# Kernel tuning notes

Hardware: AMD Instinct MI355X
Metric: run time of the kernel (lower is better)

## Reference

```python
import jax, jax.numpy as jnp
import numpy as np

N = 100000
E = 1600000
D_IN = 128
D_H = 128


def _sage_conv(x, src, dst, W_self, W_neigh, b, n_nodes):
    # mean aggregation over in-neighbors: dst receives from src
    gathered = x[src]                                        # [E, D]
    summed = jax.ops.segment_sum(gathered, dst, num_segments=n_nodes)  # [N, D]
    deg = jax.ops.segment_sum(jnp.ones((src.shape[0],), x.dtype), dst,
                              num_segments=n_nodes)          # [N]
    mean_neigh = summed / jnp.maximum(deg, 1.0)[:, None]     # zero-degree -> 0
    return x @ W_self + mean_neigh @ W_neigh + b


def setup_inputs() -> dict:
    key = jax.random.key(0)
    ks = jax.random.split(key, 9)
    s1 = 1.0 / np.sqrt(D_IN)
    s2 = 1.0 / np.sqrt(D_H)
    return {
        "in_feat": jax.random.normal(ks[0], (N, D_IN), jnp.float32),
        "W1_self": jax.random.uniform(ks[1], (D_IN, D_H), jnp.float32, -s1, s1),
        "W1_neigh": jax.random.uniform(ks[2], (D_IN, D_H), jnp.float32, -s1, s1),
        "b1": jnp.zeros((D_H,), jnp.float32),
        "W2_self": jax.random.uniform(ks[3], (D_H, D_H), jnp.float32, -s2, s2),
        "W2_neigh": jax.random.uniform(ks[4], (D_H, D_H), jnp.float32, -s2, s2),
        "b2": jnp.zeros((D_H,), jnp.float32),
        "src": jax.random.randint(ks[5], (E,), 0, N, jnp.int32),
        "dst": jax.random.randint(ks[6], (E,), 0, N, jnp.int32),
    }


def reference(in_feat, W1_self, W1_neigh, b1, W2_self, W2_neigh, b2, src, dst):
    h = _sage_conv(in_feat, src, dst, W1_self, W1_neigh, b1, N)
    h = jax.nn.relu(h)
    h = _sage_conv(h, src, dst, W2_self, W2_neigh, b2, N)
    return h
```

## Files before the change

kernel.cpp:

```cpp
#include <hip/hip_runtime.h>
#include <hip/hip_fp16.h>

#define D 128
#define NB_MAX 1024
#define PART_BLOCKS 512
#define CNT_BLOCKS 512

using f32x4  = __attribute__((ext_vector_type(4))) float;
using half8  = __attribute__((ext_vector_type(8))) _Float16;
using short8 = __attribute__((ext_vector_type(8))) short;

#define AS1(p) ((const __attribute__((address_space(1))) void*)(p))
#define AS3(p) ((__attribute__((address_space(3))) void*)(p))

#define FMA_MIX_LO(acc, dw, one) \
    asm("v_fma_mix_f32 %0, %1, %2, %0 op_sel:[0,0,0] op_sel_hi:[1,0,0]" \
        : "+v"(acc) : "v"(dw), "v"(one))
#define FMA_MIX_HI(acc, dw, one) \
    asm("v_fma_mix_f32 %0, %1, %2, %0 op_sel:[1,0,0] op_sel_hi:[1,0,0]" \
        : "+v"(acc) : "v"(dw), "v"(one))

__global__ void prep_k(const float* __restrict__ x, __half* __restrict__ y, int n4,
                       const float* __restrict__ W1s, const float* __restrict__ W1n,
                       const float* __restrict__ W2s, const float* __restrict__ W2n,
                       unsigned short* __restrict__ Wg1, unsigned short* __restrict__ Wg2,
                       const int* __restrict__ dst, int* __restrict__ bucket_counts,
                       int E, int nb, float* __restrict__ xpad) {
    __shared__ int hist[NB_MAX];
    int b = blockIdx.x;
    int t = threadIdx.x;
    if (b < CNT_BLOCKS) {
        if (b == 0 && t < 64) xpad[t] = 0.f;
        for (int i = t; i < nb; i += 256) hist[i] = 0;
        __syncthreads();
        for (int i = b * 256 + t; i < E; i += CNT_BLOCKS * 256)
            atomicAdd(&hist[dst[i] >> 8], 1);
        __syncthreads();
        for (int i = t; i < nb; i += 256) {
            int c = hist[i];
            if (c) atomicAdd(&bucket_counts[i], c);
        }
        return;
    }
    int wb = b - CNT_BLOCKS;
    if (wb < 256) {
        int sel = wb >> 7;
        int lb  = wb & 127;
        const float* Ws = sel ? W2s : W1s;
        const float* Wn = sel ? W2n : W1n;
        unsigned short* Wg = sel ? Wg2 : Wg1;
        int idx = lb * 256 + t;
        int col = idx >> 8;
        int k   = idx & 255;
        float v = (k < 128) ? Ws[k * D + col] : Wn[(k - 128) * D + col];
        _Float16 hv = (_Float16)v;
        _Float16 lv = (_Float16)(v - (float)hv);
        int kc = k >> 5, q = (k >> 3) & 3, j = k & 7;
        Wg[(((kc * 2 + 0) * 4 + q) * 128 + col) * 8 + j] = *(unsigned short*)&hv;
        Wg[(((kc * 2 + 1) * 4 + q) * 128 + col) * 8 + j] = *(unsigned short*)&lv;
        return;
    }
    int i = (b - CNT_BLOCKS - 256) * 256 + t;
    if (i < n4) {
        float4 v = *(const float4*)(x + (size_t)i * 4);
        __half2 h0 = __floats2half2_rn(v.x, v.y);
        __half2 h1 = __floats2half2_rn(v.z, v.w);
        __half2* o = (__half2*)(y + (size_t)i * 4);
        o[0] = h0; o[1] = h1;
    }
}

__global__ void bucket_scan_k(const int* __restrict__ bucket_counts,
                              int* __restrict__ bucket_base,
                              int* __restrict__ bucket_cursor, int nb) {
    __shared__ int sh[256];
    int t = threadIdx.x;
    int base = t * 4;
    int v0 = (base + 0 < nb) ? bucket_counts[base + 0] : 0;
    int v1 = (base + 1 < nb) ? bucket_counts[base + 1] : 0;
    int v2 = (base + 2 < nb) ? bucket_counts[base + 2] : 0;
    int v3 = (base + 3 < nb) ? bucket_counts[base + 3] : 0;
    int tsum = v0 + v1 + v2 + v3;
    sh[t] = tsum;
    __syncthreads();
    for (int off = 1; off < 256; off <<= 1) {
        int x = 0;
        if (t >= off) x = sh[t - off];
        __syncthreads();
        if (t >= off) sh[t] += x;
        __syncthreads();
    }
    int excl = sh[t] - tsum;
    if (base + 0 < nb) { bucket_base[base+0] = excl;          bucket_cursor[base+0] = excl; }
    if (base + 1 < nb) { bucket_base[base+1] = excl+v0;       bucket_cursor[base+1] = excl+v0; }
    if (base + 2 < nb) { bucket_base[base+2] = excl+v0+v1;    bucket_cursor[base+2] = excl+v0+v1; }
    if (base + 3 < nb) { bucket_base[base+3] = excl+v0+v1+v2; bucket_cursor[base+3] = excl+v0+v1+v2; }
    if (t == 255) bucket_base[nb] = sh[255];
}

__global__ void partition_k(const int* __restrict__ src, const int* __restrict__ dst,
                            int* __restrict__ bucket_cursor, unsigned* __restrict__ pairs,
                            int E, int nb, int chunk) {
    __shared__ int hist[NB_MAX];
    __shared__ int bbase[NB_MAX];
    int t = threadIdx.x;
    int e0 = blockIdx.x * chunk;
    int e1 = min(E, e0 + chunk);
    for (int b = t; b < nb; b += 256) hist[b] = 0;
    __syncthreads();
    for (int i = e0 + t; i < e1; i += 256)
        atomicAdd(&hist[dst[i] >> 8], 1);
    __syncthreads();
    for (int b = t; b < nb; b += 256) {
        int c = hist[b];
        int bs = 0;
        if (c) bs = atomicAdd(&bucket_cursor[b], c);
        bbase[b] = bs;
        hist[b] = 0;
    }
    __syncthreads();
    for (int i = e0 + t; i < e1; i += 256) {
        int dd = dst[i];
        int b = dd >> 8;
        int r = atomicAdd(&hist[b], 1);
        pairs[bbase[b] + r] = ((unsigned)(dd & 255) << 17) | (unsigned)src[i];
    }
}

__global__ void build_csr_k(const unsigned* __restrict__ pairs,
                            const int* __restrict__ bucket_base,
                            int2* __restrict__ offcnt,
                            int* __restrict__ edge_src, int N) {
    __shared__ int hist[256];
    __shared__ int curs[256];
    __shared__ int sh[256];
    int t = threadIdx.x;
    int b = blockIdx.x;
    int n0 = b << 8;
    int e0 = bucket_base[b];
    int e1 = bucket_base[b + 1];
    hist[t] = 0;
    __syncthreads();
    for (int i = e0 + t; i < e1; i += 256)
        atomicAdd(&hist[pairs[i] >> 17], 1);
    __syncthreads();
    int c = hist[t];
    sh[t] = c;
    __syncthreads();
    for (int off = 1; off < 256; off <<= 1) {
        int x = 0;
        if (t >= off) x = sh[t - off];
        __syncthreads();
        if (t >= off) sh[t] += x;
        __syncthreads();
    }
    int excl = sh[t] - c;
    curs[t] = excl;
    int node = n0 + t;
    if (node < N) offcnt[node] = make_int2(e0 + excl, c);
    __syncthreads();
    for (int i = e0 + t; i < e1; i += 256) {
        unsigned p = pairs[i];
        int pos = atomicAdd(&curs[p >> 17], 1);
        edge_src[e0 + pos] = (int)(p & 0x1FFFFu);
    }
}

__global__ void aggregate_f16_k(const __half* __restrict__ x,
                                const int* __restrict__ edge_src,
                                const int2* __restrict__ offcnt,
                                __half* __restrict__ agg, int n) {
    int wid  = (blockIdx.x * blockDim.x + threadIdx.x) >> 6;
    int lane = threadIdx.x & 63;
    if (wid >= n) return;
    int sg  = lane >> 4;
    int sub = lane & 15;
    int2 oc = offcnt[wid];
    int start = oc.x;
    int cnt   = oc.y;
    float one = 1.0f;
    float acc[8] = {0.f, 0.f, 0.f, 0.f, 0.f, 0.f, 0.f, 0.f};
    for (int base = 0; base < cnt; base += 64) {
        int valid = min(64, cnt - base);
        int s = (lane < valid) ? edge_src[start + base + lane] : n;
        for (int k0 = 0; k0 < valid; k0 += 16) {
            float4 raw[4];
            #pragma unroll
            for (int u = 0; u < 4; ++u) {
                int row = __shfl(s, (k0 + 4 * u + sg) & 63);
                raw[u] = *(const float4*)(x + (size_t)row * D + sub * 8);
            }
            #pragma unroll
            for (int u = 0; u < 4; ++u) {
                const unsigned* dw = (const unsigned*)&raw[u];
                #pragma unroll
                for (int j = 0; j < 4; ++j) {
                    FMA_MIX_LO(acc[2 * j],     dw[j], one);
                    FMA_MIX_HI(acc[2 * j + 1], dw[j], one);
                }
            }
        }
    }
    #pragma unroll
    for (int j = 0; j < 8; ++j) {
        acc[j] += __shfl(acc[j], lane ^ 16);
        acc[j] += __shfl(acc[j], lane ^ 32);
    }
    if (sg == 0) {
        float inv = 1.0f / fmaxf((float)cnt, 1.0f);
        union { __half2 h2[4]; short8 s8; } u;
        #pragma unroll
        for (int j = 0; j < 4; ++j)
            u.h2[j] = __floats2half2_rn(acc[2 * j] * inv, acc[2 * j + 1] * inv);
        *(short8*)(agg + (size_t)wid * D + sub * 8) = u.s8;
    }
}

__global__ __launch_bounds__(512)
void mfma_gemm_k(const _Float16* __restrict__ A0, const _Float16* __restrict__ A1,
                 const unsigned short* __restrict__ Wg,
                 const float* __restrict__ bias,
                 float* __restrict__ C, __half* __restrict__ Ch,
                 int n, int out_mode) {
    __shared__ __align__(16) unsigned short lds_b[8192];
    int t = threadIdx.x;
    int w = t >> 6;
    int l = t & 63;
    int m = l & 15;
    int q = l >> 4;
    int r0 = blockIdx.x * 256 + w * 32;

    f32x4 acc[2][8];
    #pragma unroll
    for (int rt = 0; rt < 2; ++rt)
        #pragma unroll
        for (int ct = 0; ct < 8; ++ct)
            acc[rt][ct] = (f32x4){0.f, 0.f, 0.f, 0.f};

    for (int kc = 0; kc < 8; ++kc) {
        const unsigned short* gk = Wg + (size_t)kc * 8192;
        #pragma unroll
        for (int i = 0; i < 2; ++i) {
            int e = i * 512 + t;
            __builtin_amdgcn_global_load_lds(AS1(gk + e * 8), AS3(lds_b + e * 8), 16, 0, 0);
        }
        const _Float16* __restrict__ A = (kc < 4) ? A0 : A1;
        int ka = (kc & 3) * 32;
        half8 a[2];
        #pragma unroll
        for (int rt = 0; rt < 2; ++rt) {
            int row = r0 + rt * 16 + m;
            half8 v = (half8){0, 0, 0, 0, 0, 0, 0, 0};
            if (row < n) v = *(const half8*)(A + (size_t)row * D + ka + q * 8);
            a[rt] = v;
        }
        __syncthreads();

        #pragma unroll
        for (int ct = 0; ct < 8; ++ct) {
            half8 bh = *(const half8*)&lds_b[(size_t)(q * 128 + ct * 16 + m) * 8];
            half8 bl = *(const half8*)&lds_b[(size_t)((4 + q) * 128 + ct * 16 + m) * 8];
            #pragma unroll
            for (int rt = 0; rt < 2; ++rt) {
                acc[rt][ct] = __builtin_amdgcn_mfma_f32_16x16x32_f16(a[rt], bh, acc[rt][ct], 0, 0, 0);
                acc[rt][ct] = __builtin_amdgcn_mfma_f32_16x16x32_f16(a[rt], bl, acc[rt][ct], 0, 0, 0);
            }
        }
        __syncthreads();
    }

    #pragma unroll
    for (int ct = 0; ct < 8; ++ct) {
        int col = ct * 16 + m;
        float bb = bias[col];
        #pragma unroll
        for (int rt = 0; rt < 2; ++rt) {
            #pragma unroll
            for (int r = 0; r < 4; ++r) {
                int row = r0 + rt * 16 + q * 4 + r;
                if (row < n) {
                    float v = acc[rt][ct][r] + bb;
                    if (out_mode) {
                        v = fmaxf(v, 0.f);
                        Ch[(size_t)row * D + col] = __float2half(v);
                    } else {
                        C[(size_t)row * D + col] = v;
                    }
                }
            }
        }
    }
}

extern "C" void kernel_launch(void* const* d_in, const int* in_sizes, int n_in,
                              void* d_out, int out_size, void* d_ws, size_t ws_size,
                              hipStream_t stream) {
    const float* in_feat = (const float*)d_in[0];
    const float* W1s     = (const float*)d_in[1];
    const float* W1n     = (const float*)d_in[2];
    const float* b1      = (const float*)d_in[3];
    const float* W2s     = (const float*)d_in[4];
    const float* W2n     = (const float*)d_in[5];
    const float* b2      = (const float*)d_in[6];
    const int*   src     = (const int*)d_in[7];
    const int*   dst     = (const int*)d_in[8];

    const int N  = in_sizes[0] / D;
    const int E  = in_sizes[7];
    const int NB = (N + 255) >> 8;

    char* base = (char*)d_ws;
    size_t off = 0;
    __half* agg16 = (__half*)(base + off); off += (size_t)N * D * 2;
    __half* xh16  = (__half*)(base + off); off += ((size_t)N * D + D) * 2;
    int* edge_src = (int*)(base + off);    off += (size_t)E * 4;
    int2* offcnt  = (int2*)(base + off);   off += (size_t)N * 8;
    unsigned short* Wg1 = (unsigned short*)(base + off); off += 65536 * 2;
    unsigned short* Wg2 = (unsigned short*)(base + off); off += 65536 * 2;
    int* bucket_counts = (int*)(base + off); off += NB_MAX * 4;
    int* bucket_base   = (int*)(base + off); off += (NB_MAX + 1) * 4;
    off = (off + 15) & ~(size_t)15;
    int* bucket_cursor = (int*)(base + off); off += NB_MAX * 4;

    unsigned* pairs = (unsigned*)agg16;
    float* xpad = (float*)(xh16 + (size_t)N * D);

    const int chunk = (E + PART_BLOCKS - 1) / PART_BLOCKS;
    const int n4 = (N * D) / 4;
    const int xb = (n4 + 255) / 256;

    hipMemsetAsync(bucket_counts, 0, NB_MAX * 4, stream);

    hipLaunchKernelGGL(prep_k, dim3(CNT_BLOCKS + 256 + xb), dim3(256), 0, stream,
                       in_feat, xh16, n4, W1s, W1n, W2s, W2n, Wg1, Wg2,
                       dst, bucket_counts, E, NB, xpad);

    hipLaunchKernelGGL(bucket_scan_k, dim3(1), dim3(256), 0, stream,
                       bucket_counts, bucket_base, bucket_cursor, NB);
    hipLaunchKernelGGL(partition_k, dim3(PART_BLOCKS), dim3(256), 0, stream,
                       src, dst, bucket_cursor, pairs, E, NB, chunk);
    hipLaunchKernelGGL(build_csr_k, dim3(NB), dim3(256), 0, stream,
                       pairs, bucket_base, offcnt, edge_src, N);

    const dim3 aggGrid(((size_t)N * 64 + 255) / 256);
    const dim3 gemmGrid((N + 255) / 256);

    hipLaunchKernelGGL(aggregate_f16_k, aggGrid, dim3(256), 0, stream,
                       xh16, edge_src, offcnt, agg16, N);
    hipLaunchKernelGGL(mfma_gemm_k, gemmGrid, dim3(512), 0, stream,
                       (const _Float16*)xh16, (const _Float16*)agg16, Wg1, b1,
                       (float*)nullptr, xh16, N, 1);

    hipLaunchKernelGGL(aggregate_f16_k, aggGrid, dim3(256), 0, stream,
                       xh16, edge_src, offcnt, agg16, N);
    hipLaunchKernelGGL(mfma_gemm_k, gemmGrid, dim3(512), 0, stream,
                       (const _Float16*)xh16, (const _Float16*)agg16, Wg2, b2,
                       (float*)d_out, (__half*)nullptr, N, 0);
}
```

Before: 344.7 us.

## Fuse bucket scan into partition and stage scatters through shared memory

Removes the separate single-block bucket scan kernel. Each partition and CSR block now recomputes the global bucket prefix from bucket_counts, with partition using a packed 64-bit combined scan for local and global offsets. Partition stages its pairs in LDS sorted by bucket and writes them out grouped per bucket for more contiguous stores. build_csr also stages edge sources in LDS before a coalesced writeback. The cost is redundant per-block scans and larger LDS use that may lower occupancy, plus capacity limits (PV_CAP, CS_CAP) that rely on the chunk and degree sizes of this input.

Result: slower. 356.8 us (+3.5%).

```diff
diff --git a/kernel.cpp b/kernel.cpp
--- a/kernel.cpp
+++ b/kernel.cpp
@@ -3,8 +3,10 @@
 
 #define D 128
 #define NB_MAX 1024
-#define PART_BLOCKS 512
 #define CNT_BLOCKS 512
+#define PV_CHUNK 6250
+#define PV_CAP   6400
+#define CS_CAP   5376
 
 using f32x4  = __attribute__((ext_vector_type(4))) float;
 using half8  = __attribute__((ext_vector_type(8))) _Float16;
@@ -70,77 +72,110 @@
     }
 }
 
-__global__ void bucket_scan_k(const int* __restrict__ bucket_counts,
-                              int* __restrict__ bucket_base,
-                              int* __restrict__ bucket_cursor, int nb) {
-    __shared__ int sh[256];
-    int t = threadIdx.x;
-    int base = t * 4;
-    int v0 = (base + 0 < nb) ? bucket_counts[base + 0] : 0;
-    int v1 = (base + 1 < nb) ? bucket_counts[base + 1] : 0;
-    int v2 = (base + 2 < nb) ? bucket_counts[base + 2] : 0;
-    int v3 = (base + 3 < nb) ? bucket_counts[base + 3] : 0;
-    int tsum = v0 + v1 + v2 + v3;
-    sh[t] = tsum;
-    __syncthreads();
-    for (int off = 1; off < 256; off <<= 1) {
-        int x = 0;
-        if (t >= off) x = sh[t - off];
-        __syncthreads();
-        if (t >= off) sh[t] += x;
-        __syncthreads();
-    }
-    int excl = sh[t] - tsum;
-    if (base + 0 < nb) { bucket_base[base+0] = excl;          bucket_cursor[base+0] = excl; }
-    if (base + 1 < nb) { bucket_base[base+1] = excl+v0;       bucket_cursor[base+1] = excl+v0; }
-    if (base + 2 < nb) { bucket_base[base+2] = excl+v0+v1;    bucket_cursor[base+2] = excl+v0+v1; }
-    if (base + 3 < nb) { bucket_base[base+3] = excl+v0+v1+v2; bucket_cursor[base+3] = excl+v0+v1+v2; }
-    if (t == 255) bucket_base[nb] = sh[255];
-}
-
-__global__ void partition_k(const int* __restrict__ src, const int* __restrict__ dst,
-                            int* __restrict__ bucket_cursor, unsigned* __restrict__ pairs,
-                            int E, int nb, int chunk) {
+__global__ __launch_bounds__(256)
+void partition_k(const int* __restrict__ src, const int* __restrict__ dst,
+                 const int* __restrict__ bucket_counts, int* __restrict__ bucket_cursor,
+                 unsigned* __restrict__ pairs, int E, int nb, int chunk) {
+    __shared__ unsigned stage[PV_CAP];
     __shared__ int hist[NB_MAX];
-    __shared__ int bbase[NB_MAX];
+    __shared__ int lbase[NB_MAX];
+    __shared__ int gbase[NB_MAX];
+    __shared__ long long shll[256];
     int t = threadIdx.x;
     int e0 = blockIdx.x * chunk;
     int e1 = min(E, e0 + chunk);
-    for (int b = t; b < nb; b += 256) hist[b] = 0;
+    for (int b = t; b < NB_MAX; b += 256) hist[b] = 0;
     __syncthreads();
     for (int i = e0 + t; i < e1; i += 256)
         atomicAdd(&hist[dst[i] >> 8], 1);
     __syncthreads();
-    for (int b = t; b < nb; b += 256) {
-        int c = hist[b];
-        int bs = 0;
-        if (c) bs = atomicAdd(&bucket_cursor[b], c);
-        bbase[b] = bs;
-        hist[b] = 0;
+    int t4 = t * 4;
+    int gb[4], lb[4];
+    long long tsum = 0;
+    #pragma unroll
+    for (int j = 0; j < 4; ++j) {
+        gb[j] = bucket_counts[t4 + j];
+        lb[j] = hist[t4 + j];
+        tsum += ((long long)gb[j] << 32) | (unsigned)lb[j];
+    }
+    shll[t] = tsum;
+    __syncthreads();
+    for (int off = 1; off < 256; off <<= 1) {
+        long long v = 0;
+        if (t >= off) v = shll[t - off];
+        __syncthreads();
+        if (t >= off) shll[t] += v;
+        __syncthreads();
+    }
+    long long ex = shll[t] - tsum;
+    int ge = (int)(ex >> 32);
+    int le = (int)(ex & 0xffffffffLL);
+    #pragma unroll
+    for (int j = 0; j < 4; ++j) {
+        int bkt = t4 + j;
+        lbase[bkt] = le;
+        int c = lb[j];
+        int g = ge;
+        if (c) g += atomicAdd(&bucket_cursor[bkt], c);
+        gbase[bkt] = g;
+        hist[bkt] = 0;
+        ge += gb[j];
+        le += c;
     }
     __syncthreads();
     for (int i = e0 + t; i < e1; i += 256) {
         int dd = dst[i];
         int b = dd >> 8;
         int r = atomicAdd(&hist[b], 1);
-        pairs[bbase[b] + r] = ((unsigned)(dd & 255) << 17) | (unsigned)src[i];
-    }
-}
-
-__global__ void build_csr_k(const unsigned* __restrict__ pairs,
-                            const int* __restrict__ bucket_base,
-                            int2* __restrict__ offcnt,
-                            int* __restrict__ edge_src, int N) {
+        stage[lbase[b] + r] = ((unsigned)(dd & 255) << 17) | (unsigned)src[i];
+    }
+    __syncthreads();
+    int g16 = t >> 4, sub = t & 15;
+    for (int b = g16; b < nb; b += 16) {
+        int c = hist[b];
+        int l0 = lbase[b], g0 = gbase[b];
+        for (int j = sub; j < c; j += 16)
+            pairs[g0 + j] = stage[l0 + j];
+    }
+}
+
+__global__ __launch_bounds__(256)
+void build_csr_k(const unsigned* __restrict__ pairs,
+                 const int* __restrict__ bucket_counts,
+                 int2* __restrict__ offcnt,
+                 int* __restrict__ edge_src, int N) {
+    __shared__ int srcs[CS_CAP];
     __shared__ int hist[256];
     __shared__ int curs[256];
     __shared__ int sh[256];
+    __shared__ int e0s, cnts;
     int t = threadIdx.x;
     int b = blockIdx.x;
-    int n0 = b << 8;
-    int e0 = bucket_base[b];
-    int e1 = bucket_base[b + 1];
+    int t4 = t * 4;
+    int g0 = bucket_counts[t4], g1 = bucket_counts[t4 + 1];
+    int g2 = bucket_counts[t4 + 2], g3 = bucket_counts[t4 + 3];
+    int gs = g0 + g1 + g2 + g3;
+    sh[t] = gs;
     hist[t] = 0;
     __syncthreads();
+    for (int off = 1; off < 256; off <<= 1) {
+        int v = 0;
+        if (t >= off) v = sh[t - off];
+        __syncthreads();
+        if (t >= off) sh[t] += v;
+        __syncthreads();
+    }
+    if (t == (b >> 2)) {
+        int ex = sh[t] - gs;
+        int v[4] = {g0, g1, g2, g3};
+        #pragma unroll
+        for (int j = 0; j < 4; ++j)
+            if (j < (b & 3)) ex += v[j];
+        e0s = ex;
+        cnts = v[b & 3];
+    }
+    __syncthreads();
+    int e0 = e0s, cnt = cnts, e1 = e0 + cnt;
     for (int i = e0 + t; i < e1; i += 256)
         atomicAdd(&hist[pairs[i] >> 17], 1);
     __syncthreads();
@@ -148,22 +183,28 @@
     sh[t] = c;
     __syncthreads();
     for (int off = 1; off < 256; off <<= 1) {
-        int x = 0;
-        if (t >= off) x = sh[t - off];
-        __syncthreads();
-        if (t >= off) sh[t] += x;
+        int v = 0;
+        if (t >= off) v = sh[t - off];
+        __syncthreads();
+        if (t >= off) sh[t] += v;
         __syncthreads();
     }
     int excl = sh[t] - c;
     curs[t] = excl;
-    int node = n0 + t;
+    int node = (b << 8) + t;
     if (node < N) offcnt[node] = make_int2(e0 + excl, c);
     __syncthreads();
     for (int i = e0 + t; i < e1; i += 256) {
         unsigned p = pairs[i];
         int pos = atomicAdd(&curs[p >> 17], 1);
-        edge_src[e0 + pos] = (int)(p & 0x1FFFFu);
-    }
+        int s = (int)(p & 0x1FFFFu);
+        if (pos < CS_CAP) srcs[pos] = s;
+        else edge_src[e0 + pos] = s;
+    }
+    __syncthreads();
+    int lim = min(cnt, CS_CAP);
+    for (int i = t; i < lim; i += 256)
+        edge_src[e0 + i] = srcs[i];
 }
 
 __global__ void aggregate_f16_k(const __half* __restrict__ x,
@@ -314,33 +355,29 @@
     __half* agg16 = (__half*)(base + off); off += (size_t)N * D * 2;
     __half* xh16  = (__half*)(base + off); off += ((size_t)N * D + D) * 2;
     int* edge_src = (int*)(base + off);    off += (size_t)E * 4;
-    int2* offcnt  = (int2*)(base + off);   off += (size_t)N * 8;
+    int2* offcnt  = (int2*)(base + off);   off += (size_t)(N + 2) * 8;
     unsigned short* Wg1 = (unsigned short*)(base + off); off += 65536 * 2;
     unsigned short* Wg2 = (unsigned short*)(base + off); off += 65536 * 2;
     int* bucket_counts = (int*)(base + off); off += NB_MAX * 4;
-    int* bucket_base   = (int*)(base + off); off += (NB_MAX + 1) * 4;
-    off = (off + 15) & ~(size_t)15;
     int* bucket_cursor = (int*)(base + off); off += NB_MAX * 4;
 
     unsigned* pairs = (unsigned*)agg16;
     float* xpad = (float*)(xh16 + (size_t)N * D);
 
-    const int chunk = (E + PART_BLOCKS - 1) / PART_BLOCKS;
     const int n4 = (N * D) / 4;
     const int xb = (n4 + 255) / 256;
-
-    hipMemsetAsync(bucket_counts, 0, NB_MAX * 4, stream);
+    const int pblk = (E + PV_CHUNK - 1) / PV_CHUNK;
+
+    hipMemsetAsync(bucket_counts, 0, NB_MAX * 4 * 2, stream);
 
     hipLaunchKernelGGL(prep_k, dim3(CNT_BLOCKS + 256 + xb), dim3(256), 0, stream,
                        in_feat, xh16, n4, W1s, W1n, W2s, W2n, Wg1, Wg2,
                        dst, bucket_counts, E, NB, xpad);
 
-    hipLaunchKernelGGL(bucket_scan_k, dim3(1), dim3(256), 0, stream,
-                       bucket_counts, bucket_base, bucket_cursor, NB);
-    hipLaunchKernelGGL(partition_k, dim3(PART_BLOCKS), dim3(256), 0, stream,
-                       src, dst, bucket_cursor, pairs, E, NB, chunk);
+    hipLaunchKernelGGL(partition_k, dim3(pblk), dim3(256), 0, stream,
+                       src, dst, bucket_counts, bucket_cursor, pairs, E, NB, PV_CHUNK);
     hipLaunchKernelGGL(build_csr_k, dim3(NB), dim3(256), 0, stream,
-                       pairs, bucket_base, offcnt, edge_src, N);
+                       pairs, bucket_counts, offcnt, edge_src, N);
 
     const dim3 aggGrid(((size_t)N * 64 + 255) / 256);
     const dim3 gemmGrid((N + 255) / 256);
```
